# Optimization experiments

Hardware: AMD Instinct MI355X
Metric: run time of the kernel (lower is better)

The kernel has to match this reference:

```python
import jax, jax.numpy as jnp
import numpy as np

D_K = 64
SCALE = D_K ** (-0.5)
B, H, S = 2, 16, 2048


def setup_inputs() -> dict:
    key = jax.random.key(0)
    kq, kk, kv = jax.random.split(key, 3)
    q = jax.random.normal(kq, (B, H, S, D_K), dtype=jnp.float32)
    k = jax.random.normal(kk, (B, H, S, D_K), dtype=jnp.float32)
    v = jax.random.normal(kv, (B, H, S, D_K), dtype=jnp.float32)
    # causal mask: True means masked (matches torch masked_fill semantics)
    mask = jnp.triu(jnp.ones((S, S), dtype=bool), k=1)[None, None]  # [1,1,S,S]
    return {"q": q, "k": k, "v": v, "mask": mask}


def reference(q, k, v, mask) -> jnp.ndarray:
    # scores = q @ k^T  -> [B,H,S,S]
    scores = jnp.einsum("bhqd,bhkd->bhqk", q, k)
    # masked_fill(mask, -inf), then scale (as written in the source),
    # then softmax over the key axis. -inf * scale stays -inf.
    scores = jnp.where(mask, -jnp.inf, scores)
    attn = jax.nn.softmax(SCALE * scores, axis=-1)
    return jnp.einsum("bhqk,bhkd->bhqd", attn, v)
```

## Files before the change

### kernel.cpp

```cpp
#include <hip/hip_runtime.h>
#include <hip/hip_bf16.h>
#include <math.h>


constexpr int S  = 2048;
constexpr int D  = 64;
constexpr int BH = 32;
constexpr float SCALE = 0.125f;
constexpr float LOG2E = 1.4426950408889634f;
constexpr float QPRE  = SCALE * LOG2E;
constexpr int PSTR = 72;

typedef __attribute__((ext_vector_type(8))) short bf16x8;
typedef __attribute__((ext_vector_type(4))) short bf16x4;
typedef __attribute__((ext_vector_type(4))) float f32x4;

#if __has_builtin(__builtin_amdgcn_mfma_f32_16x16x16bf16_1k)
#define HAS_MFMA_1K 1
#else
#define HAS_MFMA_1K 0
#endif

#if __has_builtin(__builtin_amdgcn_exp2f)
#define EXP2F(x) __builtin_amdgcn_exp2f(x)
#else
#define EXP2F(x) exp2f(x)
#endif

__device__ __forceinline__ short f2bf(float x) {
    union { __hip_bfloat16 b; short s; } u; u.b = __float2bfloat16(x); return u.s;
}

__device__ __forceinline__ void gload_lds16(const void* g, void* lds) {
    __builtin_amdgcn_global_load_lds(
        (const __attribute__((address_space(1))) unsigned int*)g,
        (__attribute__((address_space(3))) unsigned int*)lds, 16, 0, 0);
}

__global__ __launch_bounds__(256) void preconv_25993142075924(
    const float* __restrict__ Kg, const float* __restrict__ Vg,
    short* __restrict__ Kb, short* __restrict__ VT)
{
    const int kt = blockIdx.x, bh = blockIdx.y, tid = threadIdx.x;
    __shared__ float lt[64 * 65];
    const float* kp = Kg + (size_t)bh * S * D;
    const float* vp = Vg + (size_t)bh * S * D;
    short* kb = Kb + (size_t)bh * S * D;
    short* vt = VT + (size_t)bh * D * S;
    #pragma unroll
    for (int e = 0; e < 4; ++e) {
        int idx = (tid + e * 256) * 4;
        int r = idx >> 6, c = idx & 63;
        f32x4 k4 = *(const f32x4*)(kp + (size_t)(kt * 64 + r) * D + c);
        bf16x4 kb4;
        kb4[0] = f2bf(k4[0]); kb4[1] = f2bf(k4[1]);
        kb4[2] = f2bf(k4[2]); kb4[3] = f2bf(k4[3]);
        *(bf16x4*)(kb + (size_t)(kt * 64 + r) * D + c) = kb4;
        f32x4 v4 = *(const f32x4*)(vp + (size_t)(kt * 64 + r) * D + c);
        lt[(c + 0) * 65 + r] = v4[0];
        lt[(c + 1) * 65 + r] = v4[1];
        lt[(c + 2) * 65 + r] = v4[2];
        lt[(c + 3) * 65 + r] = v4[3];
    }
    __syncthreads();
    #pragma unroll
    for (int e = 0; e < 2; ++e) {
        int tt = tid + e * 256;
        int d  = tt >> 3;
        int j0 = (tt & 7) * 8;
        bf16x8 o;
        #pragma unroll
        for (int jj = 0; jj < 8; ++jj)
            o[jj] = f2bf(lt[d * 65 + j0 + jj]);
        *(bf16x8*)(vt + (size_t)d * S + kt * 64 + j0) = o;
    }
}

__global__ __launch_bounds__(256, 3) void attn_fwd_v19_25993142075924(
    const float* __restrict__ Qg, const short* __restrict__ Kb,
    const short* __restrict__ VT, float* __restrict__ Og)
{
    const int bh  = blockIdx.x;
    const int qb  = 31 - (int)blockIdx.y;
    const int tid = threadIdx.x;
    const int wv  = tid >> 6;
    const int ln  = tid & 63;
    const int c16 = ln & 15;
    const int qd  = ln >> 4;

    const int q0  = qb * 64 + wv * 16;
    const int nkt = qb + 1;

    __shared__ __align__(16) short lk[2][64 * 64];
    __shared__ __align__(16) short lv[2][64 * 64];
#if !HAS_MFMA_1K
    __shared__ __align__(16) short lp[4 * 16 * PSTR];
    short* lpw = lp + wv * 16 * PSTR;
#endif

    const float* qp = Qg + (size_t)bh * S * D;
    const short* kp = Kb + (size_t)bh * S * D;
    const short* vp = VT + (size_t)bh * D * S;
    float*       op = Og + (size_t)bh * S * D;

    const int srow0 = wv * 16 + (ln >> 3);
    const int sgrp0 = (ln & 7) ^ (srow0 & 7);
    const int srow1 = srow0 + 8;
    const int sgrp1 = (ln & 7) ^ (srow1 & 7);

    bf16x8 qf[2];
    {
        const float* src = qp + (size_t)(q0 + c16) * D + qd * 8;
        #pragma unroll
        for (int khf = 0; khf < 2; ++khf) {
            f32x4 a = *(const f32x4*)(src + khf * 32);
            f32x4 b = *(const f32x4*)(src + khf * 32 + 4);
            bf16x8 f;
            f[0] = f2bf(a[0] * QPRE); f[1] = f2bf(a[1] * QPRE);
            f[2] = f2bf(a[2] * QPRE); f[3] = f2bf(a[3] * QPRE);
            f[4] = f2bf(b[0] * QPRE); f[5] = f2bf(b[1] * QPRE);
            f[6] = f2bf(b[2] * QPRE); f[7] = f2bf(b[3] * QPRE);
            qf[khf] = f;
        }
    }

    f32x4 oacc[4] = {{0,0,0,0},{0,0,0,0},{0,0,0,0},{0,0,0,0}};
    float lsum = 0.f;

    gload_lds16(kp + (size_t)srow0 * D + sgrp0 * 8, &lk[0][(wv * 16 + 0) * 64]);
    gload_lds16(vp + (size_t)srow0 * S + sgrp0 * 8, &lv[0][(wv * 16 + 0) * 64]);
    gload_lds16(kp + (size_t)srow1 * D + sgrp1 * 8, &lk[0][(wv * 16 + 8) * 64]);
    gload_lds16(vp + (size_t)srow1 * S + sgrp1 * 8, &lv[0][(wv * 16 + 8) * 64]);
    __syncthreads();

    auto step = [&](int kt_, int cur) __attribute__((always_inline)) {
        bf16x8 kf0[4], kf1[4];
        #pragma unroll
        for (int nt = 0; nt < 4; ++nt) {
            const int row = nt * 16 + c16;
            kf0[nt] = *(const bf16x8*)&lk[cur][row * 64 + ((0 + qd) ^ (row & 7)) * 8];
            kf1[nt] = *(const bf16x8*)&lk[cur][row * 64 + ((4 + qd) ^ (row & 7)) * 8];
        }

        if (kt_ + 1 < nkt) {
            const int nxt = cur ^ 1;
            const size_t kb0 = (size_t)(kt_ + 1) * 64;
            gload_lds16(kp + (kb0 + srow0) * D + sgrp0 * 8, &lk[nxt][(wv * 16 + 0) * 64]);
            gload_lds16(vp + (size_t)srow0 * S + kb0 + sgrp0 * 8, &lv[nxt][(wv * 16 + 0) * 64]);
            gload_lds16(kp + (kb0 + srow1) * D + sgrp1 * 8, &lk[nxt][(wv * 16 + 8) * 64]);
            gload_lds16(vp + (size_t)srow1 * S + kb0 + sgrp1 * 8, &lv[nxt][(wv * 16 + 8) * 64]);
        }

#if HAS_MFMA_1K
        bf16x4 vf[4][4];
        #pragma unroll
        for (int dt = 0; dt < 4; ++dt) {
            const int row = dt * 16 + c16;
            #pragma unroll
            for (int nt = 0; nt < 4; ++nt) {
                const int gl = nt * 2 + (qd >> 1);
                const int gp = gl ^ (c16 & 7);
                vf[dt][nt] = *(const bf16x4*)&lv[cur][row * 64 + gp * 8 + (qd & 1) * 4];
            }
        }
#endif

        float t[4][4];
        __builtin_amdgcn_s_setprio(1);
        #pragma unroll
        for (int nt = 0; nt < 4; ++nt) {
            f32x4 acc = {0,0,0,0};
            acc = __builtin_amdgcn_mfma_f32_16x16x32_bf16(kf0[nt], qf[0], acc, 0, 0, 0);
            acc = __builtin_amdgcn_mfma_f32_16x16x32_bf16(kf1[nt], qf[1], acc, 0, 0, 0);
            t[nt][0] = acc[0]; t[nt][1] = acc[1]; t[nt][2] = acc[2]; t[nt][3] = acc[3];
        }
        __builtin_amdgcn_s_setprio(0);

        if (kt_ == qb) {
            #pragma unroll
            for (int nt = 0; nt < 4; ++nt) {
                #pragma unroll
                for (int r = 0; r < 4; ++r) {
                    int key = kt_ * 64 + nt * 16 + qd * 4 + r;
                    if (key > q0 + c16) t[nt][r] = -INFINITY;
                }
            }
        }

#if HAS_MFMA_1K
        __builtin_amdgcn_s_setprio(1);
        #pragma unroll
        for (int nt = 0; nt < 4; ++nt) {
            float p0 = EXP2F(t[nt][0]);
            float p1 = EXP2F(t[nt][1]);
            float p2 = EXP2F(t[nt][2]);
            float p3 = EXP2F(t[nt][3]);
            lsum += (p0 + p1) + (p2 + p3);
            bf16x4 pf;
            pf[0] = f2bf(p0); pf[1] = f2bf(p1);
            pf[2] = f2bf(p2); pf[3] = f2bf(p3);
            #pragma unroll
            for (int dt = 0; dt < 4; ++dt)
                oacc[dt] = __builtin_amdgcn_mfma_f32_16x16x16bf16_1k(
                    vf[dt][nt], pf, oacc[dt], 0, 0, 0);
        }
        __builtin_amdgcn_s_setprio(0);
#else
        #pragma unroll
        for (int nt = 0; nt < 4; ++nt)
            #pragma unroll
            for (int r = 0; r < 4; ++r) {
                float pv = EXP2F(t[nt][r]);
                lsum += pv;
                lpw[c16 * PSTR + nt * 16 + qd * 4 + r] = f2bf(pv);
            }
        bf16x8 pf2[2];
        #pragma unroll
        for (int khf = 0; khf < 2; ++khf)
            pf2[khf] = *(const bf16x8*)&lpw[c16 * PSTR + khf * 32 + qd * 8];
        #pragma unroll
        for (int dt = 0; dt < 4; ++dt) {
            const int row = dt * 16 + c16;
            #pragma unroll
            for (int khf = 0; khf < 2; ++khf) {
                const int g = (khf * 4 + qd) ^ (row & 7);
                bf16x8 vf8 = *(const bf16x8*)&lv[cur][row * 64 + g * 8];
                oacc[dt] = __builtin_amdgcn_mfma_f32_16x16x32_bf16(vf8, pf2[khf], oacc[dt], 0, 0, 0);
            }
        }
#endif

        __syncthreads();
    };

    int kt = 0;
    for (; kt + 1 < nkt; kt += 2) {
        step(kt, 0);
        step(kt + 1, 1);
    }
    if (kt < nkt) step(kt, 0);

    float s = lsum;
    s += __shfl_xor(s, 16);
    s += __shfl_xor(s, 32);
    const float inv = 1.0f / s;
    float* dst = op + (size_t)(q0 + c16) * D;
    #pragma unroll
    for (int dt = 0; dt < 4; ++dt) {
        f32x4 o;
        o[0] = oacc[dt][0] * inv; o[1] = oacc[dt][1] * inv;
        o[2] = oacc[dt][2] * inv; o[3] = oacc[dt][3] * inv;
        *(f32x4*)(dst + dt * 16 + qd * 4) = o;
    }
}

__global__ __launch_bounds__(256) void attn_fwd_v1_25993142075924(
    const float* __restrict__ Qg, const float* __restrict__ Kg,
    const float* __restrict__ Vg, float* __restrict__ Og)
{
    constexpr int KSTR = 72;
    constexpr int BQ = 64, BK = 64;
    const int qt  = blockIdx.x;
    const int bh  = blockIdx.y;
    const int tid = threadIdx.x;
    const int wv  = tid >> 6;
    const int ln  = tid & 63;
    const int c16 = ln & 15;
    const int qd  = ln >> 4;

    __shared__ __align__(16) __hip_bfloat16 lk [BK][KSTR];
    __shared__ __align__(16) __hip_bfloat16 lvt[D ][KSTR];
    __shared__ __align__(16) __hip_bfloat16 lp [4][16][KSTR];

    const size_t hoff = (size_t)bh * S * D;
    const float* qp = Qg + hoff;
    const float* kp = Kg + hoff;
    const float* vp = Vg + hoff;
    float*       op = Og + hoff;
    const int q0 = qt * BQ;

    bf16x8 qf[2];
    {
        const float* src = qp + (size_t)(q0 + wv*16 + c16) * D + qd*8;
        #pragma unroll
        for (int kh = 0; kh < 2; ++kh) {
            f32x4 a = *(const f32x4*)(src + kh*32);
            f32x4 b = *(const f32x4*)(src + kh*32 + 4);
            bf16x8 f;
            f[0]=f2bf(a[0]*QPRE); f[1]=f2bf(a[1]*QPRE); f[2]=f2bf(a[2]*QPRE); f[3]=f2bf(a[3]*QPRE);
            f[4]=f2bf(b[0]*QPRE); f[5]=f2bf(b[1]*QPRE); f[6]=f2bf(b[2]*QPRE); f[7]=f2bf(b[3]*QPRE);
            qf[kh] = f;
        }
    }

    f32x4 oacc[4] = {{0,0,0,0},{0,0,0,0},{0,0,0,0},{0,0,0,0}};
    float mrun[4] = {-INFINITY,-INFINITY,-INFINITY,-INFINITY};
    float lrun[4] = {0.f,0.f,0.f,0.f};

    const int nkt = qt + 1;
    for (int kt = 0; kt < nkt; ++kt) {
        __syncthreads();
        #pragma unroll
        for (int e = 0; e < 4; ++e) {
            int idx = (tid + e*256) * 4;
            int row = idx >> 6, col = idx & 63;
            f32x4 k4 = *(const f32x4*)(kp + (size_t)(kt*BK + row)*D + col);
            bf16x4 kb;
            kb[0]=f2bf(k4[0]); kb[1]=f2bf(k4[1]); kb[2]=f2bf(k4[2]); kb[3]=f2bf(k4[3]);
            *(bf16x4*)&lk[row][col] = kb;
            f32x4 v4 = *(const f32x4*)(vp + (size_t)(kt*BK + row)*D + col);
            lvt[col+0][row] = __float2bfloat16(v4[0]);
            lvt[col+1][row] = __float2bfloat16(v4[1]);
            lvt[col+2][row] = __float2bfloat16(v4[2]);
            lvt[col+3][row] = __float2bfloat16(v4[3]);
        }
        __syncthreads();

        float t[4][4];
        #pragma unroll
        for (int nt = 0; nt < 4; ++nt) {
            f32x4 acc = {0,0,0,0};
            #pragma unroll
            for (int kh = 0; kh < 2; ++kh) {
                bf16x8 kf = *(const bf16x8*)&lk[nt*16 + c16][kh*32 + qd*8];
                acc = __builtin_amdgcn_mfma_f32_16x16x32_bf16(qf[kh], kf, acc, 0, 0, 0);
            }
            #pragma unroll
            for (int r = 0; r < 4; ++r) t[nt][r] = acc[r];
        }
        if (kt == nkt - 1) {
            #pragma unroll
            for (int nt = 0; nt < 4; ++nt) {
                int j = kt*BK + nt*16 + c16;
                #pragma unroll
                for (int r = 0; r < 4; ++r)
                    if (j > q0 + wv*16 + qd*4 + r) t[nt][r] = -INFINITY;
            }
        }

        float pval[4][4];
        #pragma unroll
        for (int r = 0; r < 4; ++r) {
            float tm = fmaxf(fmaxf(t[0][r], t[1][r]), fmaxf(t[2][r], t[3][r]));
            tm = fmaxf(tm, __shfl_xor(tm, 1));
            tm = fmaxf(tm, __shfl_xor(tm, 2));
            tm = fmaxf(tm, __shfl_xor(tm, 4));
            tm = fmaxf(tm, __shfl_xor(tm, 8));
            float mnew  = fmaxf(mrun[r], tm);
            float alpha = exp2f(mrun[r] - mnew);
            mrun[r] = mnew;
            float rs = 0.f;
            #pragma unroll
            for (int nt = 0; nt < 4; ++nt) {
                float pv = exp2f(t[nt][r] - mnew);
                pval[nt][r] = pv;
                rs += pv;
            }
            rs += __shfl_xor(rs, 1);
            rs += __shfl_xor(rs, 2);
            rs += __shfl_xor(rs, 4);
            rs += __shfl_xor(rs, 8);
            lrun[r] = lrun[r] * alpha + rs;
            #pragma unroll
            for (int dt = 0; dt < 4; ++dt) oacc[dt][r] *= alpha;
        }

        #pragma unroll
        for (int nt = 0; nt < 4; ++nt)
            #pragma unroll
            for (int r = 0; r < 4; ++r)
                lp[wv][qd*4 + r][nt*16 + c16] = __float2bfloat16(pval[nt][r]);
        bf16x8 pf[2];
        #pragma unroll
        for (int kh = 0; kh < 2; ++kh)
            pf[kh] = *(const bf16x8*)&lp[wv][c16][kh*32 + qd*8];

        #pragma unroll
        for (int dt = 0; dt < 4; ++dt) {
            #pragma unroll
            for (int kh = 0; kh < 2; ++kh) {
                bf16x8 vf = *(const bf16x8*)&lvt[dt*16 + c16][kh*32 + qd*8];
                oacc[dt] = __builtin_amdgcn_mfma_f32_16x16x32_bf16(pf[kh], vf, oacc[dt], 0, 0, 0);
            }
        }
    }

    #pragma unroll
    for (int r = 0; r < 4; ++r) {
        float inv = 1.0f / lrun[r];
        float* dst = op + (size_t)(q0 + wv*16 + qd*4 + r) * D;
        #pragma unroll
        for (int dt = 0; dt < 4; ++dt)
            dst[dt*16 + c16] = oacc[dt][r] * inv;
    }
}

extern "C" void kernel_launch(void* const* d_in, const int* in_sizes, int n_in,
                              void* d_out, int out_size, void* d_ws, size_t ws_size,
                              hipStream_t stream) {
    const float* q = (const float*)d_in[0];
    const float* k = (const float*)d_in[1];
    const float* v = (const float*)d_in[2];
    float* out = (float*)d_out;
    const size_t elems = (size_t)BH * S * D;
    const size_t need  = 2 * elems * sizeof(short);
    if (ws_size >= need) {
        short* Kb = (short*)d_ws;
        short* VT = Kb + elems;
        preconv_25993142075924<<<dim3(S / 64, BH), 256, 0, stream>>>(k, v, Kb, VT);
        attn_fwd_v19_25993142075924<<<dim3(BH, 32), 256, 0, stream>>>(q, Kb, VT, out);
    } else {
        attn_fwd_v1_25993142075924<<<dim3(S / 64, BH), 256, 0, stream>>>(q, k, v, out);
    }
}
```

Measured before the change: 132.3 us.

## Split waves into 2x2 query/key halves with LDS reduction of partial outputs

Each wave now handles 32 query rows against half of the 64-key tile, instead of 16 query rows against the whole tile. The aim is to reuse each K/V fragment read from LDS across two query groups, which cuts LDS read traffic per MFMA. The cost is an end-of-kernel LDS reduction of the partial outputs and row sums between wave pairs, plus more accumulator registers. The non-1k-MFMA fallback path inside the fast kernel is removed, and without the 1k MFMA builtin the launcher falls back to the v1 kernel.

```diff
diff --git a/kernel.cpp b/kernel.cpp
--- a/kernel.cpp
+++ b/kernel.cpp
@@ -9,7 +9,6 @@
 constexpr float SCALE = 0.125f;
 constexpr float LOG2E = 1.4426950408889634f;
 constexpr float QPRE  = SCALE * LOG2E;
-constexpr int PSTR = 72;
 
 typedef __attribute__((ext_vector_type(8))) short bf16x8;
 typedef __attribute__((ext_vector_type(4))) short bf16x4;
@@ -76,7 +75,8 @@
     }
 }
 
-__global__ __launch_bounds__(256, 3) void attn_fwd_v19_25993142075924(
+#if HAS_MFMA_1K
+__global__ __launch_bounds__(256, 3) void attn_fwd_v21_25993142075924(
     const float* __restrict__ Qg, const short* __restrict__ Kb,
     const short* __restrict__ VT, float* __restrict__ Og)
 {
@@ -87,16 +87,14 @@
     const int ln  = tid & 63;
     const int c16 = ln & 15;
     const int qd  = ln >> 4;
-
-    const int q0  = qb * 64 + wv * 16;
+    const int qh  = wv >> 1;
+    const int kh  = wv & 1;
+
+    const int q0  = qb * 64 + qh * 32;
     const int nkt = qb + 1;
 
     __shared__ __align__(16) short lk[2][64 * 64];
     __shared__ __align__(16) short lv[2][64 * 64];
-#if !HAS_MFMA_1K
-    __shared__ __align__(16) short lp[4 * 16 * PSTR];
-    short* lpw = lp + wv * 16 * PSTR;
-#endif
 
     const float* qp = Qg + (size_t)bh * S * D;
     const short* kp = Kb + (size_t)bh * S * D;
@@ -108,9 +106,10 @@
     const int srow1 = srow0 + 8;
     const int sgrp1 = (ln & 7) ^ (srow1 & 7);
 
-    bf16x8 qf[2];
-    {
-        const float* src = qp + (size_t)(q0 + c16) * D + qd * 8;
+    bf16x8 qf[2][2];
+    #pragma unroll
+    for (int qg = 0; qg < 2; ++qg) {
+        const float* src = qp + (size_t)(q0 + qg * 16 + c16) * D + qd * 8;
         #pragma unroll
         for (int khf = 0; khf < 2; ++khf) {
             f32x4 a = *(const f32x4*)(src + khf * 32);
@@ -120,12 +119,13 @@
             f[2] = f2bf(a[2] * QPRE); f[3] = f2bf(a[3] * QPRE);
             f[4] = f2bf(b[0] * QPRE); f[5] = f2bf(b[1] * QPRE);
             f[6] = f2bf(b[2] * QPRE); f[7] = f2bf(b[3] * QPRE);
-            qf[khf] = f;
-        }
-    }
-
-    f32x4 oacc[4] = {{0,0,0,0},{0,0,0,0},{0,0,0,0},{0,0,0,0}};
-    float lsum = 0.f;
+            qf[qg][khf] = f;
+        }
+    }
+
+    f32x4 oacc[2][4] = {{{0,0,0,0},{0,0,0,0},{0,0,0,0},{0,0,0,0}},
+                        {{0,0,0,0},{0,0,0,0},{0,0,0,0},{0,0,0,0}}};
+    float lsum[2] = {0.f, 0.f};
 
     gload_lds16(kp + (size_t)srow0 * D + sgrp0 * 8, &lk[0][(wv * 16 + 0) * 64]);
     gload_lds16(vp + (size_t)srow0 * S + sgrp0 * 8, &lv[0][(wv * 16 + 0) * 64]);
@@ -134,12 +134,12 @@
     __syncthreads();
 
     auto step = [&](int kt_, int cur) __attribute__((always_inline)) {
-        bf16x8 kf0[4], kf1[4];
-        #pragma unroll
-        for (int nt = 0; nt < 4; ++nt) {
-            const int row = nt * 16 + c16;
-            kf0[nt] = *(const bf16x8*)&lk[cur][row * 64 + ((0 + qd) ^ (row & 7)) * 8];
-            kf1[nt] = *(const bf16x8*)&lk[cur][row * 64 + ((4 + qd) ^ (row & 7)) * 8];
+        bf16x8 kf[2][2];
+        #pragma unroll
+        for (int nt = 0; nt < 2; ++nt) {
+            const int row = kh * 32 + nt * 16 + c16;
+            kf[nt][0] = *(const bf16x8*)&lk[cur][row * 64 + ((0 + qd) ^ (row & 7)) * 8];
+            kf[nt][1] = *(const bf16x8*)&lk[cur][row * 64 + ((4 + qd) ^ (row & 7)) * 8];
         }
 
         if (kt_ + 1 < nkt) {
@@ -151,84 +151,65 @@
             gload_lds16(vp + (size_t)srow1 * S + kb0 + sgrp1 * 8, &lv[nxt][(wv * 16 + 8) * 64]);
         }
 
-#if HAS_MFMA_1K
-        bf16x4 vf[4][4];
+        bf16x4 vf[4][2];
         #pragma unroll
         for (int dt = 0; dt < 4; ++dt) {
             const int row = dt * 16 + c16;
             #pragma unroll
-            for (int nt = 0; nt < 4; ++nt) {
-                const int gl = nt * 2 + (qd >> 1);
+            for (int nt = 0; nt < 2; ++nt) {
+                const int gl = kh * 4 + nt * 2 + (qd >> 1);
                 const int gp = gl ^ (c16 & 7);
                 vf[dt][nt] = *(const bf16x4*)&lv[cur][row * 64 + gp * 8 + (qd & 1) * 4];
             }
         }
-#endif
-
-        float t[4][4];
+
+        float t[2][2][4];
         __builtin_amdgcn_s_setprio(1);
         #pragma unroll
-        for (int nt = 0; nt < 4; ++nt) {
-            f32x4 acc = {0,0,0,0};
-            acc = __builtin_amdgcn_mfma_f32_16x16x32_bf16(kf0[nt], qf[0], acc, 0, 0, 0);
-            acc = __builtin_amdgcn_mfma_f32_16x16x32_bf16(kf1[nt], qf[1], acc, 0, 0, 0);
-            t[nt][0] = acc[0]; t[nt][1] = acc[1]; t[nt][2] = acc[2]; t[nt][3] = acc[3];
+        for (int qg = 0; qg < 2; ++qg) {
+            #pragma unroll
+            for (int nt = 0; nt < 2; ++nt) {
+                f32x4 acc = {0,0,0,0};
+                acc = __builtin_amdgcn_mfma_f32_16x16x32_bf16(kf[nt][0], qf[qg][0], acc, 0, 0, 0);
+                acc = __builtin_amdgcn_mfma_f32_16x16x32_bf16(kf[nt][1], qf[qg][1], acc, 0, 0, 0);
+                t[qg][nt][0] = acc[0]; t[qg][nt][1] = acc[1];
+                t[qg][nt][2] = acc[2]; t[qg][nt][3] = acc[3];
+            }
         }
         __builtin_amdgcn_s_setprio(0);
 
         if (kt_ == qb) {
             #pragma unroll
-            for (int nt = 0; nt < 4; ++nt) {
+            for (int qg = 0; qg < 2; ++qg)
                 #pragma unroll
-                for (int r = 0; r < 4; ++r) {
-                    int key = kt_ * 64 + nt * 16 + qd * 4 + r;
-                    if (key > q0 + c16) t[nt][r] = -INFINITY;
-                }
-            }
-        }
-
-#if HAS_MFMA_1K
+                for (int nt = 0; nt < 2; ++nt)
+                    #pragma unroll
+                    for (int r = 0; r < 4; ++r) {
+                        int key = kt_ * 64 + kh * 32 + nt * 16 + qd * 4 + r;
+                        if (key > q0 + qg * 16 + c16) t[qg][nt][r] = -INFINITY;
+                    }
+        }
+
         __builtin_amdgcn_s_setprio(1);
         #pragma unroll
-        for (int nt = 0; nt < 4; ++nt) {
-            float p0 = EXP2F(t[nt][0]);
-            float p1 = EXP2F(t[nt][1]);
-            float p2 = EXP2F(t[nt][2]);
-            float p3 = EXP2F(t[nt][3]);
-            lsum += (p0 + p1) + (p2 + p3);
-            bf16x4 pf;
-            pf[0] = f2bf(p0); pf[1] = f2bf(p1);
-            pf[2] = f2bf(p2); pf[3] = f2bf(p3);
-            #pragma unroll
-            for (int dt = 0; dt < 4; ++dt)
-                oacc[dt] = __builtin_amdgcn_mfma_f32_16x16x16bf16_1k(
-                    vf[dt][nt], pf, oacc[dt], 0, 0, 0);
+        for (int qg = 0; qg < 2; ++qg) {
+            #pragma unroll
+            for (int nt = 0; nt < 2; ++nt) {
+                float p0 = EXP2F(t[qg][nt][0]);
+                float p1 = EXP2F(t[qg][nt][1]);
+                float p2 = EXP2F(t[qg][nt][2]);
+                float p3 = EXP2F(t[qg][nt][3]);
+                lsum[qg] += (p0 + p1) + (p2 + p3);
+                bf16x4 pf;
+                pf[0] = f2bf(p0); pf[1] = f2bf(p1);
+                pf[2] = f2bf(p2); pf[3] = f2bf(p3);
+                #pragma unroll
+                for (int dt = 0; dt < 4; ++dt)
+                    oacc[qg][dt] = __builtin_amdgcn_mfma_f32_16x16x16bf16_1k(
+                        vf[dt][nt], pf, oacc[qg][dt], 0, 0, 0);
+            }
         }
         __builtin_amdgcn_s_setprio(0);
-#else
-        #pragma unroll
-        for (int nt = 0; nt < 4; ++nt)
-            #pragma unroll
-            for (int r = 0; r < 4; ++r) {
-                float pv = EXP2F(t[nt][r]);
-                lsum += pv;
-                lpw[c16 * PSTR + nt * 16 + qd * 4 + r] = f2bf(pv);
-            }
-        bf16x8 pf2[2];
-        #pragma unroll
-        for (int khf = 0; khf < 2; ++khf)
-            pf2[khf] = *(const bf16x8*)&lpw[c16 * PSTR + khf * 32 + qd * 8];
-        #pragma unroll
-        for (int dt = 0; dt < 4; ++dt) {
-            const int row = dt * 16 + c16;
-            #pragma unroll
-            for (int khf = 0; khf < 2; ++khf) {
-                const int g = (khf * 4 + qd) ^ (row & 7);
-                bf16x8 vf8 = *(const bf16x8*)&lv[cur][row * 64 + g * 8];
-                oacc[dt] = __builtin_amdgcn_mfma_f32_16x16x32_bf16(vf8, pf2[khf], oacc[dt], 0, 0, 0);
-            }
-        }
-#endif
 
         __syncthreads();
     };
@@ -240,19 +221,51 @@
     }
     if (kt < nkt) step(kt, 0);
 
-    float s = lsum;
-    s += __shfl_xor(s, 16);
-    s += __shfl_xor(s, 32);
-    const float inv = 1.0f / s;
-    float* dst = op + (size_t)(q0 + c16) * D;
-    #pragma unroll
-    for (int dt = 0; dt < 4; ++dt) {
-        f32x4 o;
-        o[0] = oacc[dt][0] * inv; o[1] = oacc[dt][1] * inv;
-        o[2] = oacc[dt][2] * inv; o[3] = oacc[dt][3] * inv;
-        *(f32x4*)(dst + dt * 16 + qd * 4) = o;
-    }
-}
+    lsum[0] += __shfl_xor(lsum[0], 16); lsum[0] += __shfl_xor(lsum[0], 32);
+    lsum[1] += __shfl_xor(lsum[1], 16); lsum[1] += __shfl_xor(lsum[1], 32);
+
+    float* scr  = (float*)&lk[0][0];
+    float* scrl = (float*)&lv[0][0];
+    const int sbase = (qh * 64 + ln) * 32;
+    if (kh == 1) {
+        #pragma unroll
+        for (int c = 0; c < 8; ++c) {
+            const int cc = c ^ (ln & 7);
+            *(f32x4*)&scr[sbase + cc * 4] = oacc[c >> 2][c & 3];
+        }
+        if (qd == 0) {
+            scrl[qh * 32 + c16]      = lsum[0];
+            scrl[qh * 32 + 16 + c16] = lsum[1];
+        }
+    }
+    __syncthreads();
+    if (kh == 0) {
+        #pragma unroll
+        for (int c = 0; c < 8; ++c) {
+            const int cc = c ^ (ln & 7);
+            f32x4 p = *(const f32x4*)&scr[sbase + cc * 4];
+            oacc[c >> 2][c & 3][0] += p[0];
+            oacc[c >> 2][c & 3][1] += p[1];
+            oacc[c >> 2][c & 3][2] += p[2];
+            oacc[c >> 2][c & 3][3] += p[3];
+        }
+        const float inv0 = 1.0f / (lsum[0] + scrl[qh * 32 + c16]);
+        const float inv1 = 1.0f / (lsum[1] + scrl[qh * 32 + 16 + c16]);
+        #pragma unroll
+        for (int qg = 0; qg < 2; ++qg) {
+            const float inv = qg ? inv1 : inv0;
+            float* dst = op + (size_t)(q0 + qg * 16 + c16) * D;
+            #pragma unroll
+            for (int dt = 0; dt < 4; ++dt) {
+                f32x4 o;
+                o[0] = oacc[qg][dt][0] * inv; o[1] = oacc[qg][dt][1] * inv;
+                o[2] = oacc[qg][dt][2] * inv; o[3] = oacc[qg][dt][3] * inv;
+                *(f32x4*)(dst + dt * 16 + qd * 4) = o;
+            }
+        }
+    }
+}
+#endif
 
 __global__ __launch_bounds__(256) void attn_fwd_v1_25993142075924(
     const float* __restrict__ Qg, const float* __restrict__ Kg,
@@ -404,12 +417,15 @@
     float* out = (float*)d_out;
     const size_t elems = (size_t)BH * S * D;
     const size_t need  = 2 * elems * sizeof(short);
+#if HAS_MFMA_1K
     if (ws_size >= need) {
         short* Kb = (short*)d_ws;
         short* VT = Kb + elems;
         preconv_25993142075924<<<dim3(S / 64, BH), 256, 0, stream>>>(k, v, Kb, VT);
-        attn_fwd_v19_25993142075924<<<dim3(BH, 32), 256, 0, stream>>>(q, Kb, VT, out);
-    } else {
-        attn_fwd_v1_25993142075924<<<dim3(S / 64, BH), 256, 0, stream>>>(q, k, v, out);
-    }
-}
+        attn_fwd_v21_25993142075924<<<dim3(BH, 32), 256, 0, stream>>>(q, Kb, VT, out);
+        return;
+    }
+#endif
+    (void)need;
+    attn_fwd_v1_25993142075924<<<dim3(S / 64, BH), 256, 0, stream>>>(q, k, v, out);
+}
```

Result: slower. 269.4 us (+103.6%).
